# Optimization experiments

Measured on AMD Instinct MI355X. Metric: run time of the kernel, lower is better.

Reference implementation:

```python
import jax, jax.numpy as jnp
import numpy as np


def setup_inputs() -> dict:
    key = jax.random.key(0)
    k1, k2 = jax.random.split(key)
    TOKENS, IN, OUT = 32768, 1024, 1024
    x = jax.random.normal(k1, (TOKENS, IN), dtype=jnp.float32)
    # weight init: uniform(-1, 1) over [out_features, in_features]
    weight = jax.random.uniform(k2, (OUT, IN), dtype=jnp.float32, minval=-1.0, maxval=1.0)
    b = jnp.zeros((OUT,), dtype=jnp.float32)
    return {"x": x, "weight": weight, "b": b}


def reference(x, weight, b):
    # ternary quantization: sign() zeros out exact zeros; mask keeps nonzeros
    sign = jnp.sign(weight)
    mask = (weight != 0).astype(x.dtype)
    w_q = sign * mask  # [out, in], values in {-1, 0, 1}
    # F.linear: x @ w_q.T + b
    return jnp.einsum("ti,oi->to", x, w_q) + b
```

## Files before the change

kernel.cpp:

```cpp
#include <hip/hip_runtime.h>
#include <hip/hip_bf16.h>


typedef int   i32x4 __attribute__((ext_vector_type(4)));
typedef float f32x4 __attribute__((ext_vector_type(4)));

#define BM 128
#define BN 128
#define BK 64

__device__ __forceinline__ void async16(const void* gptr, void* lptr) {
    __builtin_amdgcn_global_load_lds(
        (const __attribute__((address_space(1))) unsigned int*)gptr,
        (__attribute__((address_space(3))) unsigned int*)lptr,
        16, 0, 0);
}

__device__ __forceinline__ int clamp127(int v) {
    v = v > 127 ? 127 : v;
    v = v < -127 ? -127 : v;
    return v;
}

__device__ __forceinline__ int pack4(int a, int b, int c, int d) {
    return (a & 255) | ((b & 255) << 8) | ((c & 255) << 16) | ((d & 255) << 24);
}

__device__ __forceinline__ int sgnb(float v) {
    return (v > 0.0f) ? 1 : ((v < 0.0f) ? -1 : 0);
}


__global__ __launch_bounds__(256)
void quant_pre(const float* __restrict__ x, const float* __restrict__ w,
               signed char* __restrict__ xq, signed char* __restrict__ wq,
               float* __restrict__ scales, int M, int K, long nw, int xblocks) {
    const int tid = threadIdx.x;

    if ((int)blockIdx.x >= xblocks) {
        long i = ((long)(blockIdx.x - xblocks) * 256 + tid) * 8;
        if (i + 8 > nw) return;
        const float4* p = (const float4*)(w + i);
        float4 a = p[0];
        float4 b = p[1];
        int lo = pack4(sgnb(a.x), sgnb(a.y), sgnb(a.z), sgnb(a.w));
        int hi = pack4(sgnb(b.x), sgnb(b.y), sgnb(b.z), sgnb(b.w));
        int2 v; v.x = lo; v.y = hi;
        *(int2*)(wq + i) = v;
        return;
    }

    const int wv   = tid >> 6;
    const int lane = tid & 63;
    const int row  = blockIdx.x * 4 + wv;
    if (row >= M) return;

    const float* xr = x + (long)row * K;
    const int chunks = K >> 8;
    float4 v[8];
    float m = 0.0f;
#pragma unroll
    for (int q = 0; q < 8; ++q) {
        if (q >= chunks) break;
        v[q] = *(const float4*)(xr + q * 256 + lane * 4);
        m = fmaxf(m, fmaxf(fmaxf(fabsf(v[q].x), fabsf(v[q].y)),
                           fmaxf(fabsf(v[q].z), fabsf(v[q].w))));
    }
#pragma unroll
    for (int off = 32; off > 0; off >>= 1)
        m = fmaxf(m, __shfl_xor(m, off, 64));

    const float inv = (m > 0.0f) ? (127.0f / m) : 0.0f;
    int* qr = (int*)(xq + (long)row * K);
#pragma unroll
    for (int q = 0; q < 8; ++q) {
        if (q >= chunks) break;
        int a = clamp127(__float2int_rn(v[q].x * inv));
        int b = clamp127(__float2int_rn(v[q].y * inv));
        int c = clamp127(__float2int_rn(v[q].z * inv));
        int d = clamp127(__float2int_rn(v[q].w * inv));
        qr[q * 64 + lane] = pack4(a, b, c, d);
    }
    if (lane == 0) scales[row] = m * (1.0f / 127.0f);
}


__global__ __launch_bounds__(256)
void gemm_i8(const signed char* __restrict__ A, const signed char* __restrict__ B,
             const float* __restrict__ scales, const float* __restrict__ bias,
             float* __restrict__ C, int M, int N, int K, int swz) {
    __shared__ __align__(16) signed char sA[BM * BK];
    __shared__ __align__(16) signed char sB[BN * BK];

    const int tid  = threadIdx.x;
    const int lane = tid & 63;
    const int wave = tid >> 6;

    const int gn = N / BN;
    int mt, nt;
    if (swz) {
        const int b    = blockIdx.x;
        const int xcd  = b & 7;
        const int rest = b >> 3;
        nt = rest % gn;
        mt = (rest / gn) * 8 + xcd;
    } else {
        nt = blockIdx.x % gn;
        mt = blockIdx.x / gn;
    }
    const int bm = mt * BM;
    const int bn = nt * BN;

    const int wrow = (wave >> 1) * 64;
    const int wcol = (wave & 1) * 64;
    const int quad = lane >> 4;
    const int l16  = lane & 15;

    i32x4 acc[4][4] = {};

    const int row0  = tid >> 2;
    const int col16 = (tid & 3) * 16;
    const signed char* pa0 = A + (long)(bm + row0) * K + col16;
    const signed char* pa1 = pa0 + (long)64 * K;
    const signed char* pb0 = B + (long)(bn + row0) * K + col16;
    const signed char* pb1 = pb0 + (long)64 * K;

    for (int k0 = 0; k0 < K; k0 += BK) {
        async16(pa0 + k0, (char*)sA + tid * 16);
        async16(pa1 + k0, (char*)sA + (256 + tid) * 16);
        async16(pb0 + k0, (char*)sB + tid * 16);
        async16(pb1 + k0, (char*)sB + (256 + tid) * 16);
        __syncthreads();

        i32x4 af[4], bfr[4];
#pragma unroll
        for (int i = 0; i < 4; ++i) {
            af[i]  = *(const i32x4*)&sA[(wrow + i * 16 + l16) * BK + quad * 16];
            bfr[i] = *(const i32x4*)&sB[(wcol + i * 16 + l16) * BK + quad * 16];
        }
#pragma unroll
        for (int i = 0; i < 4; ++i)
#pragma unroll
            for (int j = 0; j < 4; ++j)
                acc[i][j] = __builtin_amdgcn_mfma_i32_16x16x64_i8(af[i], bfr[j], acc[i][j], 0, 0, 0);

        __syncthreads();
    }

#pragma unroll
    for (int j = 0; j < 4; ++j) {
        const int col = bn + wcol + j * 16 + l16;
        const float bv = bias[col];
#pragma unroll
        for (int i = 0; i < 4; ++i) {
            const int rbase = bm + wrow + i * 16 + quad * 4;
#pragma unroll
            for (int r = 0; r < 4; ++r) {
                const int row = rbase + r;
                C[(long)row * N + col] = (float)acc[i][j][r] * scales[row] + bv;
            }
        }
    }
}


__device__ __forceinline__ float signf(float v) {
    return (v > 0.0f) ? 1.0f : ((v < 0.0f) ? -1.0f : 0.0f);
}

__global__ void fallback_kernel(const float* __restrict__ x, const float* __restrict__ w,
                                const float* __restrict__ b, float* __restrict__ out,
                                int M, int N, int K) {
    long o = (long)blockIdx.x * blockDim.x + threadIdx.x;
    if (o >= (long)M * N) return;
    int t = (int)(o / N);
    int n = (int)(o % N);
    const float* xr = x + (long)t * K;
    const float* wr = w + (long)n * K;
    float s = 0.0f;
    for (int k = 0; k < K; ++k) s += xr[k] * signf(wr[k]);
    out[o] = s + b[n];
}


extern "C" void kernel_launch(void* const* d_in, const int* in_sizes, int n_in,
                              void* d_out, int out_size, void* d_ws, size_t ws_size,
                              hipStream_t stream) {
    const float* x = (const float*)d_in[0];
    const float* w = (const float*)d_in[1];
    const float* b = (const float*)d_in[2];
    float* out = (float*)d_out;

    const int N = in_sizes[2];
    const int K = in_sizes[1] / N;
    const int M = in_sizes[0] / K;

    const long nx = (long)M * K;
    const long nw = (long)N * K;
    const size_t need = (size_t)nx + (size_t)nw + (size_t)M * 4 + 64;

    const bool fast = (M % BM == 0) && (N % BN == 0) && (K % BK == 0) &&
                      (K % 256 == 0) && (K <= 2048) && (nw % 2048 == 0) &&
                      (ws_size >= need);

    if (!fast) {
        long total = (long)M * N;
        int blocks = (int)((total + 255) / 256);
        fallback_kernel<<<blocks, 256, 0, stream>>>(x, w, b, out, M, N, K);
        return;
    }

    signed char* xq = (signed char*)d_ws;
    signed char* wq = xq + nx;
    float* scales   = (float*)(wq + nw);

    const int xblocks = M / 4;
    const int wblocks = (int)(nw / 2048);
    quant_pre<<<xblocks + wblocks, 256, 0, stream>>>(x, w, xq, wq, scales, M, K, nw, xblocks);

    const int gm = M / BM, gn = N / BN;
    const int swz = (gm % 8 == 0) ? 1 : 0;
    gemm_i8<<<gm * gn, 256, 0, stream>>>(xq, wq, scales, b, out, M, N, K, swz);
}
```

Measured before the change: 286.5 us.

## Fuse activation quantization into GEMM with whole-K A tile resident in LDS

Adds a fused kernel that loads a 128-row block of fp32 activations, quantizes each row to int8 with its scale directly into LDS (padded pitch), then sweeps all N tiles with two wave groups computing two 128-column tiles concurrently using int8 MFMA. Weight signs are produced by a separate small kernel. This removes the global write and reread of the quantized activations and the standalone quantize pass. In exchange, the large LDS footprint limits occupancy to one block per CU, and the single-buffered B loads with per-step barriers may expose latency.

```diff
diff --git a/kernel.cpp b/kernel.cpp
--- a/kernel.cpp
+++ b/kernel.cpp
@@ -3,11 +3,8 @@
 
 
 typedef int   i32x4 __attribute__((ext_vector_type(4)));
-typedef float f32x4 __attribute__((ext_vector_type(4)));
-
-#define BM 128
-#define BN 128
-#define BK 64
+
+#define APITCH 1040
 
 __device__ __forceinline__ void async16(const void* gptr, void* lptr) {
     __builtin_amdgcn_global_load_lds(
@@ -30,31 +27,149 @@
     return (v > 0.0f) ? 1 : ((v < 0.0f) ? -1 : 0);
 }
 
+__device__ __forceinline__ int quant4(const float4 v, float inv) {
+    return pack4(clamp127(__float2int_rn(v.x * inv)),
+                 clamp127(__float2int_rn(v.y * inv)),
+                 clamp127(__float2int_rn(v.z * inv)),
+                 clamp127(__float2int_rn(v.w * inv)));
+}
+
+
+__global__ __launch_bounds__(256)
+void w_sign(const float* __restrict__ w, signed char* __restrict__ wq, long nw) {
+    long i = ((long)blockIdx.x * 256 + threadIdx.x) * 8;
+    if (i + 8 > nw) return;
+    const float4* p = (const float4*)(w + i);
+    float4 a = p[0];
+    float4 b = p[1];
+    int2 v;
+    v.x = pack4(sgnb(a.x), sgnb(a.y), sgnb(a.z), sgnb(a.w));
+    v.y = pack4(sgnb(b.x), sgnb(b.y), sgnb(b.z), sgnb(b.w));
+    *(int2*)(wq + i) = v;
+}
+
+
+__global__ __launch_bounds__(512, 2)
+void fused_gemm(const float* __restrict__ x, const signed char* __restrict__ Bq,
+                const float* __restrict__ bias, float* __restrict__ C,
+                int M, int N) {
+    constexpr int K = 1024;
+    __shared__ __align__(16) signed char sA[128 * APITCH];
+    __shared__ __align__(16) signed char sB[16384];
+    __shared__ float sScale[128];
+
+    const int tid  = threadIdx.x;
+    const int wave = tid >> 6;
+    const int lane = tid & 63;
+    const int bm   = blockIdx.x * 128;
+
+    {
+        const float* xb = x + (long)bm * K;
+#pragma unroll 2
+        for (int rr = 0; rr < 16; ++rr) {
+            const int row = wave * 16 + rr;
+            const float4* p = (const float4*)(xb + (long)row * K + lane * 16);
+            float4 v0 = p[0], v1 = p[1], v2 = p[2], v3 = p[3];
+            float m = fmaxf(fmaxf(fabsf(v0.x), fabsf(v0.y)), fmaxf(fabsf(v0.z), fabsf(v0.w)));
+            m = fmaxf(m, fmaxf(fmaxf(fabsf(v1.x), fabsf(v1.y)), fmaxf(fabsf(v1.z), fabsf(v1.w))));
+            m = fmaxf(m, fmaxf(fmaxf(fabsf(v2.x), fabsf(v2.y)), fmaxf(fabsf(v2.z), fabsf(v2.w))));
+            m = fmaxf(m, fmaxf(fmaxf(fabsf(v3.x), fabsf(v3.y)), fmaxf(fabsf(v3.z), fabsf(v3.w))));
+#pragma unroll
+            for (int off = 32; off > 0; off >>= 1)
+                m = fmaxf(m, __shfl_xor(m, off, 64));
+            const float inv = (m > 0.0f) ? (127.0f / m) : 0.0f;
+            i32x4 q;
+            q[0] = quant4(v0, inv);
+            q[1] = quant4(v1, inv);
+            q[2] = quant4(v2, inv);
+            q[3] = quant4(v3, inv);
+            *(i32x4*)&sA[(long)row * APITCH + lane * 16] = q;
+            if (lane == 0) sScale[row] = m * (1.0f / 127.0f);
+        }
+    }
+    __syncthreads();
+
+    const int grp  = wave >> 2;
+    const int w4   = wave & 3;
+    const int wrow = (w4 >> 1) * 64;
+    const int wcol = (w4 & 1) * 64;
+    const int quad = lane >> 4;
+    const int l16  = lane & 15;
+
+    const int tt   = tid >> 8;
+    const int idx  = tid & 255;
+    const int srow = idx >> 2;
+    const int sc   = idx & 3;
+    const int c0   = (sc ^ (srow & 3)) * 16;
+
+    for (int nt = 0; nt < N / 128; nt += 2) {
+        i32x4 acc[4][4] = {};
+        const signed char* bq = Bq + (long)((nt + tt) * 128 + srow) * K + c0;
+        for (int k0 = 0; k0 < K; k0 += 64) {
+            async16(bq + k0, (char*)sB + tt * 8192 + idx * 16);
+            async16(bq + (long)64 * K + k0, (char*)sB + tt * 8192 + 4096 + idx * 16);
+            __syncthreads();
+
+            i32x4 af[4], bf[4];
+#pragma unroll
+            for (int i = 0; i < 4; ++i)
+                af[i] = *(const i32x4*)&sA[(long)(wrow + i * 16 + l16) * APITCH + k0 + quad * 16];
+#pragma unroll
+            for (int j = 0; j < 4; ++j) {
+                const int r2 = wcol + j * 16 + l16;
+                bf[j] = *(const i32x4*)&sB[grp * 8192 + r2 * 64 + ((quad ^ (r2 & 3)) * 16)];
+            }
+#pragma unroll
+            for (int i = 0; i < 4; ++i)
+#pragma unroll
+                for (int j = 0; j < 4; ++j)
+                    acc[i][j] = __builtin_amdgcn_mfma_i32_16x16x64_i8(af[i], bf[j], acc[i][j], 0, 0, 0);
+
+            __syncthreads();
+        }
+
+        const int bn0 = (nt + grp) * 128;
+#pragma unroll
+        for (int j = 0; j < 4; ++j) {
+            const int col = bn0 + wcol + j * 16 + l16;
+            const float bv = bias[col];
+#pragma unroll
+            for (int i = 0; i < 4; ++i) {
+                const int rl = wrow + i * 16 + quad * 4;
+#pragma unroll
+                for (int r = 0; r < 4; ++r)
+                    C[(long)(bm + rl + r) * N + col] = (float)acc[i][j][r] * sScale[rl + r] + bv;
+            }
+        }
+    }
+}
+
+
+#define BM 128
+#define BN 128
+#define BK 64
 
 __global__ __launch_bounds__(256)
 void quant_pre(const float* __restrict__ x, const float* __restrict__ w,
                signed char* __restrict__ xq, signed char* __restrict__ wq,
                float* __restrict__ scales, int M, int K, long nw, int xblocks) {
     const int tid = threadIdx.x;
-
     if ((int)blockIdx.x >= xblocks) {
         long i = ((long)(blockIdx.x - xblocks) * 256 + tid) * 8;
         if (i + 8 > nw) return;
         const float4* p = (const float4*)(w + i);
         float4 a = p[0];
         float4 b = p[1];
-        int lo = pack4(sgnb(a.x), sgnb(a.y), sgnb(a.z), sgnb(a.w));
-        int hi = pack4(sgnb(b.x), sgnb(b.y), sgnb(b.z), sgnb(b.w));
-        int2 v; v.x = lo; v.y = hi;
+        int2 v;
+        v.x = pack4(sgnb(a.x), sgnb(a.y), sgnb(a.z), sgnb(a.w));
+        v.y = pack4(sgnb(b.x), sgnb(b.y), sgnb(b.z), sgnb(b.w));
         *(int2*)(wq + i) = v;
         return;
     }
-
     const int wv   = tid >> 6;
     const int lane = tid & 63;
     const int row  = blockIdx.x * 4 + wv;
     if (row >= M) return;
-
     const float* xr = x + (long)row * K;
     const int chunks = K >> 8;
     float4 v[8];
@@ -69,33 +184,25 @@
 #pragma unroll
     for (int off = 32; off > 0; off >>= 1)
         m = fmaxf(m, __shfl_xor(m, off, 64));
-
     const float inv = (m > 0.0f) ? (127.0f / m) : 0.0f;
     int* qr = (int*)(xq + (long)row * K);
 #pragma unroll
     for (int q = 0; q < 8; ++q) {
         if (q >= chunks) break;
-        int a = clamp127(__float2int_rn(v[q].x * inv));
-        int b = clamp127(__float2int_rn(v[q].y * inv));
-        int c = clamp127(__float2int_rn(v[q].z * inv));
-        int d = clamp127(__float2int_rn(v[q].w * inv));
-        qr[q * 64 + lane] = pack4(a, b, c, d);
+        qr[q * 64 + lane] = quant4(v[q], inv);
     }
     if (lane == 0) scales[row] = m * (1.0f / 127.0f);
 }
-
 
 __global__ __launch_bounds__(256)
 void gemm_i8(const signed char* __restrict__ A, const signed char* __restrict__ B,
              const float* __restrict__ scales, const float* __restrict__ bias,
              float* __restrict__ C, int M, int N, int K, int swz) {
-    __shared__ __align__(16) signed char sA[BM * BK];
-    __shared__ __align__(16) signed char sB[BN * BK];
-
+    __shared__ __align__(16) signed char sA2[BM * BK];
+    __shared__ __align__(16) signed char sB2[BN * BK];
     const int tid  = threadIdx.x;
     const int lane = tid & 63;
     const int wave = tid >> 6;
-
     const int gn = N / BN;
     int mt, nt;
     if (swz) {
@@ -110,43 +217,36 @@
     }
     const int bm = mt * BM;
     const int bn = nt * BN;
-
     const int wrow = (wave >> 1) * 64;
     const int wcol = (wave & 1) * 64;
     const int quad = lane >> 4;
     const int l16  = lane & 15;
-
     i32x4 acc[4][4] = {};
-
     const int row0  = tid >> 2;
     const int col16 = (tid & 3) * 16;
     const signed char* pa0 = A + (long)(bm + row0) * K + col16;
     const signed char* pa1 = pa0 + (long)64 * K;
     const signed char* pb0 = B + (long)(bn + row0) * K + col16;
     const signed char* pb1 = pb0 + (long)64 * K;
-
     for (int k0 = 0; k0 < K; k0 += BK) {
-        async16(pa0 + k0, (char*)sA + tid * 16);
-        async16(pa1 + k0, (char*)sA + (256 + tid) * 16);
-        async16(pb0 + k0, (char*)sB + tid * 16);
-        async16(pb1 + k0, (char*)sB + (256 + tid) * 16);
+        async16(pa0 + k0, (char*)sA2 + tid * 16);
+        async16(pa1 + k0, (char*)sA2 + (256 + tid) * 16);
+        async16(pb0 + k0, (char*)sB2 + tid * 16);
+        async16(pb1 + k0, (char*)sB2 + (256 + tid) * 16);
         __syncthreads();
-
         i32x4 af[4], bfr[4];
 #pragma unroll
         for (int i = 0; i < 4; ++i) {
-            af[i]  = *(const i32x4*)&sA[(wrow + i * 16 + l16) * BK + quad * 16];
-            bfr[i] = *(const i32x4*)&sB[(wcol + i * 16 + l16) * BK + quad * 16];
+            af[i]  = *(const i32x4*)&sA2[(wrow + i * 16 + l16) * BK + quad * 16];
+            bfr[i] = *(const i32x4*)&sB2[(wcol + i * 16 + l16) * BK + quad * 16];
         }
 #pragma unroll
         for (int i = 0; i < 4; ++i)
 #pragma unroll
             for (int j = 0; j < 4; ++j)
                 acc[i][j] = __builtin_amdgcn_mfma_i32_16x16x64_i8(af[i], bfr[j], acc[i][j], 0, 0, 0);
-
         __syncthreads();
     }
-
 #pragma unroll
     for (int j = 0; j < 4; ++j) {
         const int col = bn + wcol + j * 16 + l16;
@@ -197,28 +297,34 @@
 
     const long nx = (long)M * K;
     const long nw = (long)N * K;
+
+    const bool fused_ok = (K == 1024) && (M % 128 == 0) && (N % 256 == 0) &&
+                          (nw % 2048 == 0) && (ws_size >= (size_t)nw + 64);
+    if (fused_ok) {
+        signed char* wq = (signed char*)d_ws;
+        w_sign<<<(int)(nw / 2048), 256, 0, stream>>>(w, wq, nw);
+        fused_gemm<<<M / 128, 512, 0, stream>>>(x, wq, b, out, M, N);
+        return;
+    }
+
     const size_t need = (size_t)nx + (size_t)nw + (size_t)M * 4 + 64;
-
-    const bool fast = (M % BM == 0) && (N % BN == 0) && (K % BK == 0) &&
-                      (K % 256 == 0) && (K <= 2048) && (nw % 2048 == 0) &&
-                      (ws_size >= need);
-
-    if (!fast) {
-        long total = (long)M * N;
-        int blocks = (int)((total + 255) / 256);
-        fallback_kernel<<<blocks, 256, 0, stream>>>(x, w, b, out, M, N, K);
+    const bool split_ok = (M % BM == 0) && (N % BN == 0) && (K % BK == 0) &&
+                          (K % 256 == 0) && (K <= 2048) && (nw % 2048 == 0) &&
+                          (ws_size >= need);
+    if (split_ok) {
+        signed char* xq = (signed char*)d_ws;
+        signed char* wq = xq + nx;
+        float* scales   = (float*)(wq + nw);
+        const int xblocks = M / 4;
+        const int wblocks = (int)(nw / 2048);
+        quant_pre<<<xblocks + wblocks, 256, 0, stream>>>(x, w, xq, wq, scales, M, K, nw, xblocks);
+        const int gm = M / BM, gn = N / BN;
+        const int swz = (gm % 8 == 0) ? 1 : 0;
+        gemm_i8<<<gm * gn, 256, 0, stream>>>(xq, wq, scales, b, out, M, N, K, swz);
         return;
     }
 
-    signed char* xq = (signed char*)d_ws;
-    signed char* wq = xq + nx;
-    float* scales   = (float*)(wq + nw);
-
-    const int xblocks = M / 4;
-    const int wblocks = (int)(nw / 2048);
-    quant_pre<<<xblocks + wblocks, 256, 0, stream>>>(x, w, xq, wq, scales, M, K, nw, xblocks);
-
-    const int gm = M / BM, gn = N / BN;
-    const int swz = (gm % 8 == 0) ? 1 : 0;
-    gemm_i8<<<gm * gn, 256, 0, stream>>>(xq, wq, scales, b, out, M, N, K, swz);
-}
+    long total = (long)M * N;
+    int blocks = (int)((total + 255) / 256);
+    fallback_kernel<<<blocks, 256, 0, stream>>>(x, w, b, out, M, N, K);
+}
```

Result: no change. 291.8 us (+1.8%).
